# Kernel tuning notes

Measured on AMD Instinct MI355X. Metric: run time of the kernel, lower is better.

Reference implementation:

```python
import jax, jax.numpy as jnp
import numpy as np

N = 50000      # nodes
E = 800000     # edges (before self loops)
IN = 256       # in_dim
HID = 32       # hidden_dim per head
H = 8          # heads layer 1
OUT = 64       # out_dim (classes)
NEG_SLOPE = 0.2  # PyG GATConv default


def gat_conv(x, ei, W, a_src, a_dst, b, heads, ch, concat):
    """PyG GATConv (eval mode, self-loops already in ei).
    x: [n, f_in], ei: [2, e] (row0=src j, row1=dst i), W: [f_in, heads*ch],
    a_src/a_dst: [heads, ch], b: [heads*ch] or [ch]."""
    n = x.shape[0]
    h = (x @ W).reshape(n, heads, ch)                      # [n, H, C]
    src, dst = ei[0], ei[1]
    alpha_src = (h * a_src).sum(-1)                        # [n, H]
    alpha_dst = (h * a_dst).sum(-1)                        # [n, H]
    e = jax.nn.leaky_relu(alpha_src[src] + alpha_dst[dst], NEG_SLOPE)  # [e, H]
    # segment softmax over incoming edges of each dst node
    emax = jax.lax.stop_gradient(jax.ops.segment_max(e, dst, num_segments=n))
    p = jnp.exp(e - emax[dst])
    denom = jax.ops.segment_sum(p, dst, num_segments=n)    # [n, H] (>0: self loops)
    alpha = p / denom[dst]                                 # [e, H]
    out = jax.ops.segment_sum(h[src] * alpha[:, :, None], dst, num_segments=n)  # [n, H, C]
    out = out.reshape(n, heads * ch) if concat else out.mean(axis=1)
    return out + b


def setup_inputs() -> dict:
    key = jax.random.key(0)
    ks = jax.random.split(key, 9)
    x = jax.random.normal(ks[0], (N, IN), jnp.float32)
    edge_index = jax.random.randint(ks[1], (2, E), 0, N, jnp.int32)
    W1 = jax.random.normal(ks[2], (IN, H * HID), jnp.float32) * 0.05
    a_src1 = jax.random.normal(ks[3], (H, HID), jnp.float32) * 0.1
    a_dst1 = jax.random.normal(ks[4], (H, HID), jnp.float32) * 0.1
    b1 = jnp.zeros((H * HID,), jnp.float32)
    W2 = jax.random.normal(ks[5], (H * HID, OUT), jnp.float32) * 0.05
    a_src2 = jax.random.normal(ks[6], (1, OUT), jnp.float32) * 0.1
    a_dst2 = jax.random.normal(ks[7], (1, OUT), jnp.float32) * 0.1
    b2 = jnp.zeros((OUT,), jnp.float32)
    return {"x": x, "edge_index": edge_index, "W1": W1, "a_src1": a_src1,
            "a_dst1": a_dst1, "b1": b1, "W2": W2, "a_src2": a_src2,
            "a_dst2": a_dst2, "b2": b2}


def reference(x, edge_index, W1, a_src1, a_dst1, b1, W2, a_src2, a_dst2, b2):
    n = x.shape[0]
    loops = jnp.arange(n, dtype=edge_index.dtype)
    ei = jnp.concatenate([edge_index, jnp.stack([loops, loops])], axis=1)  # add self loops
    h = gat_conv(x, ei, W1, a_src1, a_dst1, b1, H, HID, concat=True)
    h = jax.nn.relu(h)
    h = gat_conv(h, ei, W2, a_src2, a_dst2, b2, 1, OUT, concat=False)
    return jax.nn.log_softmax(h, axis=1)
```

## Files before the change

### kernel.cpp

```cpp
#include <hip/hip_runtime.h>
#include <math.h>

#define NNODES 50000
#define EORIG  800000
#define ETOT   850000
#define NBUCK  196
#define BSTRIDE 5120
#define P2CHUNK 4096
#define NBLK2  ((ETOT + P2CHUNK - 1)/P2CHUNK)

typedef __attribute__((ext_vector_type(8))) short bf8_t;
typedef __attribute__((ext_vector_type(4))) float f4_t;
typedef __attribute__((ext_vector_type(2))) float f2_t;

constexpr float LOG2E = 1.44269504f;

constexpr size_t align256(size_t x){ return (x + 255) & ~size_t(255); }
constexpr size_t OFF_OFFSETS = 0;
constexpr size_t OFF_DEG     = OFF_OFFSETS + align256((size_t)NNODES*4);
constexpr size_t OFF_GCUR    = OFF_DEG     + align256((size_t)NNODES*4);
constexpr size_t OFF_EPACK   = OFF_GCUR    + align256(NBUCK*4);
constexpr size_t OFF_SRC     = OFF_EPACK   + align256((size_t)NBUCK*BSTRIDE*4);
constexpr size_t OFF_AS1     = OFF_SRC     + align256((size_t)NBUCK*BSTRIDE*4);
constexpr size_t OFF_AD1     = OFF_AS1     + align256((size_t)NNODES*8*4);
constexpr size_t OFF_W1T     = OFF_AD1     + align256((size_t)NNODES*8*4);
constexpr size_t OFF_W2T     = OFF_W1T     + align256(256*256*2);
constexpr size_t OFF_H1F8    = OFF_W2T     + align256(64*256*2);
constexpr size_t OFF_OUT1B   = OFF_H1F8    + align256((size_t)NNODES*256);
constexpr size_t OFF_H2B     = OFF_H1F8;
constexpr size_t OFF_AS2     = OFF_OUT1B   + align256((size_t)NNODES*256*2);
constexpr size_t OFF_AD2     = OFF_AS2     + align256((size_t)NNODES*4);

__device__ __forceinline__ unsigned short f2bf(float f){
    union { float f; unsigned u; } v; v.f = f;
    unsigned r = v.u + 0x7FFF + ((v.u >> 16) & 1);
    return (unsigned short)(r >> 16);
}
__device__ __forceinline__ float bf2f(unsigned short s){
    union { unsigned u; float f; } v; v.u = ((unsigned)s) << 16;
    return v.f;
}


__global__ __launch_bounds__(256) void p3_part(const int* __restrict__ ei, int* __restrict__ gcur,
                                               int* __restrict__ epack){
    __shared__ int h[NBUCK];
    __shared__ int r[NBUCK];
    const int t = threadIdx.x;
    for (int i = t; i < NBUCK; i += 256){ h[i] = 0; r[i] = 0; }
    __syncthreads();
    const int base = blockIdx.x * P2CHUNK;
    int srcs[P2CHUNK/256], dsts[P2CHUNK/256];
#pragma unroll
    for (int j = 0; j < P2CHUNK/256; j++){
        int e = base + j*256 + t;
        if (e < ETOT){
            if (e < EORIG){ srcs[j] = ei[e]; dsts[j] = ei[EORIG + e]; }
            else          { srcs[j] = dsts[j] = e - EORIG; }
            atomicAdd(&h[dsts[j] >> 8], 1);
        } else dsts[j] = -1;
    }
    __syncthreads();
    for (int i = t; i < NBUCK; i += 256){
        int c = h[i];
        h[i] = c ? atomicAdd(&gcur[i], c) : 0;
    }
    __syncthreads();
#pragma unroll
    for (int j = 0; j < P2CHUNK/256; j++){
        if (dsts[j] >= 0){
            int b = dsts[j] >> 8;
            int rk = atomicAdd(&r[b], 1);
            epack[h[b] + rk] = (srcs[j] << 8) | (dsts[j] & 255);
        }
    }
}

__global__ __launch_bounds__(256) void p4_csr(const int* __restrict__ gcur, const int* __restrict__ epack,
                                              int* __restrict__ offsets, int* __restrict__ deg_g,
                                              int* __restrict__ srclist){
    __shared__ int deg[256];
    __shared__ int sm[256];
    __shared__ int cur[256];
    const int b = blockIdx.x, t = threadIdx.x;
    const int s0 = b * BSTRIDE, s1 = gcur[b];
    deg[t] = 0; __syncthreads();
    for (int i = s0 + t; i < s1; i += 256) atomicAdd(&deg[epack[i] & 255], 1);
    __syncthreads();
    int v = deg[t];
    sm[t] = v; __syncthreads();
    for (int off = 1; off < 256; off <<= 1){
        int add = (t >= off) ? sm[t-off] : 0;
        __syncthreads();
        sm[t] += add;
        __syncthreads();
    }
    int excl = sm[t] - v;
    int node = (b << 8) + t;
    if (node < NNODES){ offsets[node] = s0 + excl; deg_g[node] = v; }
    cur[t] = s0 + excl;
    __syncthreads();
    for (int i = s0 + t; i < s1; i += 256){
        int p = epack[i];
        int pos = atomicAdd(&cur[p & 255], 1);
        srclist[pos] = p >> 8;
    }
}


__global__ __launch_bounds__(256) void conv_w_k(const float* __restrict__ W1, const float* __restrict__ W2,
                                                short* __restrict__ w1t, short* __restrict__ w2t,
                                                int* __restrict__ gcur){
    int o = blockIdx.x*256 + threadIdx.x;
    if (o < NBUCK) gcur[o] = o * BSTRIDE;
    if (o < 256*256){
        int n = o >> 8, k = o & 255;
        w1t[o] = (short)f2bf(W1[k*256 + n]);
    } else {
        int o2 = o - 256*256;
        if (o2 < 64*256){
            int n = o2 >> 8, k = o2 & 255;
            w2t[o2] = (short)f2bf(W2[k*64 + n]);
        }
    }
}


__global__ __launch_bounds__(512) void gemm1_mfma(const float* __restrict__ x, const short* __restrict__ w1t,
        const float* __restrict__ a1s, const float* __restrict__ a1d,
        unsigned char* __restrict__ h1f8, float* __restrict__ as1, float* __restrict__ ad1){
    __shared__ short As[128][40];
    __shared__ short Bs[256][40];
    const int t = threadIdx.x;
    const int lane = t & 63, wave = t >> 6;
    const int wy = wave >> 2, wx = wave & 3;
    const int quad = lane >> 4, l15 = lane & 15;
    const int r0 = blockIdx.x * 128;
    const int srow = t >> 2, skoff = (t & 3) * 8;
    f4_t zero4 = {0.f,0.f,0.f,0.f};
    f4_t acc[4][4];
#pragma unroll
    for (int i=0;i<4;i++)
#pragma unroll
      for (int j=0;j<4;j++) acc[i][j] = zero4;

    for (int kk = 0; kk < 256; kk += 32){
        float4 xa0 = {0,0,0,0}, xa1 = {0,0,0,0};
        if (r0 + srow < NNODES){
            xa0 = *(const float4*)(x + (size_t)(r0+srow)*256 + kk + skoff);
            xa1 = *(const float4*)(x + (size_t)(r0+srow)*256 + kk + skoff + 4);
        }
        bf8_t b0  = *(const bf8_t*)(w1t + (size_t)(srow      )*256 + kk + skoff);
        bf8_t b1v = *(const bf8_t*)(w1t + (size_t)(srow + 128)*256 + kk + skoff);
        bf8_t a0;
        a0[0]=f2bf(xa0.x); a0[1]=f2bf(xa0.y); a0[2]=f2bf(xa0.z); a0[3]=f2bf(xa0.w);
        a0[4]=f2bf(xa1.x); a0[5]=f2bf(xa1.y); a0[6]=f2bf(xa1.z); a0[7]=f2bf(xa1.w);
        __syncthreads();
        *(bf8_t*)&As[srow     ][skoff] = a0;
        *(bf8_t*)&Bs[srow     ][skoff] = b0;
        *(bf8_t*)&Bs[srow+128][skoff] = b1v;
        __syncthreads();
        bf8_t af[4], bfr[4];
#pragma unroll
        for (int i=0;i<4;i++) af[i]  = *(const bf8_t*)&As[wy*64 + i*16 + l15][quad*8];
#pragma unroll
        for (int j=0;j<4;j++) bfr[j] = *(const bf8_t*)&Bs[wx*64 + j*16 + l15][quad*8];
#pragma unroll
        for (int i=0;i<4;i++)
#pragma unroll
          for (int j=0;j<4;j++)
            acc[i][j] = __builtin_amdgcn_mfma_f32_16x16x32_bf16(af[i], bfr[j], acc[i][j], 0,0,0);
    }
    const int colbase = wx*64;
    const int head0 = colbase >> 5;
    float cs[4], cd[4];
#pragma unroll
    for (int j=0;j<4;j++){
        cs[j] = a1s[colbase + j*16 + l15] * LOG2E;
        cd[j] = a1d[colbase + j*16 + l15] * LOG2E;
    }
#pragma unroll
    for (int i=0;i<4;i++){
        int rowb = r0 + wy*64 + i*16 + quad*4;
#pragma unroll
        for (int reg=0; reg<4; reg++){
            int row = rowb + reg;
            bool valid = row < NNODES;
            float sp0=0.f, dp0=0.f, sp1=0.f, dp1=0.f;
#pragma unroll
            for (int j=0;j<4;j++){
                float v = acc[i][j][reg];
                if (j < 2){ sp0 += v*cs[j]; dp0 += v*cd[j]; }
                else      { sp1 += v*cs[j]; dp1 += v*cd[j]; }
                if (valid){
                    unsigned enc = (unsigned)__builtin_amdgcn_cvt_pk_fp8_f32(v, v, 0, false);
                    h1f8[(size_t)row*256 + colbase + j*16 + l15] = (unsigned char)(enc & 0xffu);
                }
            }
            sp0 += __shfl_xor(sp0,1); sp0 += __shfl_xor(sp0,2); sp0 += __shfl_xor(sp0,4); sp0 += __shfl_xor(sp0,8);
            dp0 += __shfl_xor(dp0,1); dp0 += __shfl_xor(dp0,2); dp0 += __shfl_xor(dp0,4); dp0 += __shfl_xor(dp0,8);
            sp1 += __shfl_xor(sp1,1); sp1 += __shfl_xor(sp1,2); sp1 += __shfl_xor(sp1,4); sp1 += __shfl_xor(sp1,8);
            dp1 += __shfl_xor(dp1,1); dp1 += __shfl_xor(dp1,2); dp1 += __shfl_xor(dp1,4); dp1 += __shfl_xor(dp1,8);
            if (valid && l15 == 0){
                as1[row*8 + head0    ] = sp0;
                ad1[row*8 + head0    ] = dp0;
                as1[row*8 + head0 + 1] = sp1;
                ad1[row*8 + head0 + 1] = dp1;
            }
        }
    }
}


__global__ __launch_bounds__(256) void gemm2_mfma(const short* __restrict__ ab, const short* __restrict__ w2t,
        const float* __restrict__ a2s, const float* __restrict__ a2d,
        short* __restrict__ h2b, float* __restrict__ as2, float* __restrict__ ad2){
    __shared__ short As[128][40];
    __shared__ short Bs[64][40];
    const int t = threadIdx.x;
    const int lane = t & 63, wave = t >> 6;
    const int quad = lane >> 4, l15 = lane & 15;
    const int r0 = blockIdx.x * 128;
    const int srow = t >> 2, skoff = (t & 3) * 8;
    f4_t zero4 = {0.f,0.f,0.f,0.f};
    f4_t acc[2][4];
#pragma unroll
    for (int i=0;i<2;i++)
#pragma unroll
      for (int j=0;j<4;j++) acc[i][j] = zero4;

    for (int kk = 0; kk < 256; kk += 32){
        bf8_t a0 = {}, a1v = {};
        if (r0 + srow < NNODES)      a0  = *(const bf8_t*)(ab + (size_t)(r0+srow)*256 + kk + skoff);
        if (r0 + srow + 64 < NNODES) a1v = *(const bf8_t*)(ab + (size_t)(r0+srow+64)*256 + kk + skoff);
        bf8_t b0 = *(const bf8_t*)(w2t + (size_t)srow*256 + kk + skoff);
        __syncthreads();
        *(bf8_t*)&As[srow   ][skoff] = a0;
        *(bf8_t*)&As[srow+64][skoff] = a1v;
        *(bf8_t*)&Bs[srow   ][skoff] = b0;
        __syncthreads();
        bf8_t af[2], bfr[4];
#pragma unroll
        for (int i=0;i<2;i++) af[i]  = *(const bf8_t*)&As[wave*32 + i*16 + l15][quad*8];
#pragma unroll
        for (int j=0;j<4;j++) bfr[j] = *(const bf8_t*)&Bs[j*16 + l15][quad*8];
#pragma unroll
        for (int i=0;i<2;i++)
#pragma unroll
          for (int j=0;j<4;j++)
            acc[i][j] = __builtin_amdgcn_mfma_f32_16x16x32_bf16(af[i], bfr[j], acc[i][j], 0,0,0);
    }
    float cs[4], cd[4];
#pragma unroll
    for (int j=0;j<4;j++){
        cs[j] = a2s[j*16 + l15] * LOG2E;
        cd[j] = a2d[j*16 + l15] * LOG2E;
    }
#pragma unroll
    for (int i=0;i<2;i++){
        int rowb = r0 + wave*32 + i*16 + quad*4;
#pragma unroll
        for (int reg=0; reg<4; reg++){
            int row = rowb + reg;
            bool valid = row < NNODES;
            float sp=0.f, dp=0.f;
#pragma unroll
            for (int j=0;j<4;j++){
                float v = acc[i][j][reg];
                sp += v*cs[j]; dp += v*cd[j];
                if (valid) h2b[(size_t)row*64 + j*16 + l15] = (short)f2bf(v);
            }
            sp += __shfl_xor(sp,1); sp += __shfl_xor(sp,2); sp += __shfl_xor(sp,4); sp += __shfl_xor(sp,8);
            dp += __shfl_xor(dp,1); dp += __shfl_xor(dp,2); dp += __shfl_xor(dp,4); dp += __shfl_xor(dp,8);
            if (valid && l15 == 0){ as2[row] = sp; ad2[row] = dp; }
        }
    }
}


__global__ __launch_bounds__(256) void aggregate1_k(const unsigned char* __restrict__ h1f8,
        const float* __restrict__ as1, const float* __restrict__ ad1,
        const int* __restrict__ offsets, const int* __restrict__ deg_g,
        const int* __restrict__ srclist,
        const float* __restrict__ b1, short* __restrict__ out1b){
    int d = blockIdx.x*4 + (threadIdx.x >> 6);
    int lane = threadIdx.x & 63;
    if (d >= NNODES) return;
    const int head_g = lane >> 3;
    const int head_p = lane & 7;
    const int ep     = lane >> 3;
    int start = offsets[d];
    int deg = deg_g[d];
    float ad_p = ad1[d*8 + head_p];
    float denom = 0.f;
    f2_t acc01 = {0.f,0.f}, acc23 = {0.f,0.f};
    for (int w = 0; w < deg; w += 64){
        int deg_w = min(64, deg - w);
        int s_reg = srclist[start + w + min(lane, deg_w-1)];
        int ngr = (deg_w + 7) >> 3;
        auto comp_p = [&](int g)->float{
            int ei = g*8 + ep;
            int s  = __shfl(s_reg, min(ei, deg_w-1));
            float e = as1[s*8 + head_p] + ad_p;
            e = fmaxf(0.2f*e, e);
            float p = exp2f(e);
            return (ei < deg_w) ? p : 0.f;
        };
        float p_reg = comp_p(0);
        for (int g = 0; g < ngr; g++){
            float p_cur = p_reg;
            if (g + 1 < ngr) p_reg = comp_p(g+1);
#pragma unroll
            for (int e = 0; e < 8; e++){
                float pe = __shfl(p_cur, e*8 + head_g);
                int   se = __shfl(s_reg, g*8 + e);
                unsigned wv = *(const unsigned*)(h1f8 + (size_t)se*256 + lane*4);
                f2_t lo = __builtin_amdgcn_cvt_pk_f32_fp8(wv, false);
                f2_t hi = __builtin_amdgcn_cvt_pk_f32_fp8(wv, true);
                acc01 += pe*lo;
                acc23 += pe*hi;
                denom += pe;
            }
        }
    }
    float inv = 1.f / denom;
    float4 bv = *(const float4*)(b1 + lane*4);
    ushort4 us;
    us.x = f2bf(fmaxf(acc01[0]*inv + bv.x, 0.f));
    us.y = f2bf(fmaxf(acc01[1]*inv + bv.y, 0.f));
    us.z = f2bf(fmaxf(acc23[0]*inv + bv.z, 0.f));
    us.w = f2bf(fmaxf(acc23[1]*inv + bv.w, 0.f));
    *(ushort4*)(out1b + (size_t)d*256 + lane*4) = us;
}

__global__ __launch_bounds__(256) void aggregate2_k(const unsigned short* __restrict__ h2b,
        const float* __restrict__ as2, const float* __restrict__ ad2,
        const int* __restrict__ offsets, const int* __restrict__ deg_g,
        const int* __restrict__ srclist,
        const float* __restrict__ b2, float* __restrict__ out){
    int d = blockIdx.x*4 + (threadIdx.x >> 6);
    int lane = threadIdx.x & 63;
    if (d >= NNODES) return;
    int start = offsets[d];
    int deg = deg_g[d];
    float ad_v = ad2[d];
    float denom = 0.f, acc = 0.f;
    for (int w = 0; w < deg; w += 64){
        int deg_w = min(64, deg - w);
        int s_reg = srclist[start + w + min(lane, deg_w-1)];
        float ev = as2[s_reg] + ad_v;
        ev = fmaxf(0.2f*ev, ev);
        float p_lane = (lane < deg_w) ? exp2f(ev) : 0.f;
        int ngr = (deg_w + 7) >> 3;
        for (int g = 0; g < ngr; g++){
#pragma unroll
            for (int e2 = 0; e2 < 8; e2++){
                int ee = g*8 + e2;
                float pe = __shfl(p_lane, ee);
                int   se = __shfl(s_reg, ee);
                float hv = bf2f(h2b[(size_t)se*64 + lane]);
                acc += pe*hv;
                denom += pe;
            }
        }
    }
    float v = acc/denom + b2[lane];
    float mx = v;
#pragma unroll
    for (int off = 1; off < 64; off <<= 1) mx = fmaxf(mx, __shfl_xor(mx, off));
    float ex = __expf(v - mx);
    float ss = ex;
#pragma unroll
    for (int off = 1; off < 64; off <<= 1) ss += __shfl_xor(ss, off);
    out[(size_t)d*64 + lane] = v - mx - __logf(ss);
}


extern "C" void kernel_launch(void* const* d_in, const int* in_sizes, int n_in,
                              void* d_out, int out_size, void* d_ws, size_t ws_size,
                              hipStream_t stream){
    const float* x      = (const float*)d_in[0];
    const int*   ei     = (const int*)  d_in[1];
    const float* W1     = (const float*)d_in[2];
    const float* a_src1 = (const float*)d_in[3];
    const float* a_dst1 = (const float*)d_in[4];
    const float* b1     = (const float*)d_in[5];
    const float* W2     = (const float*)d_in[6];
    const float* a_src2 = (const float*)d_in[7];
    const float* a_dst2 = (const float*)d_in[8];
    const float* b2     = (const float*)d_in[9];

    char* ws = (char*)d_ws;
    int*   offsets = (int*)  (ws + OFF_OFFSETS);
    int*   deg_g   = (int*)  (ws + OFF_DEG);
    int*   gcur    = (int*)  (ws + OFF_GCUR);
    int*   epack   = (int*)  (ws + OFF_EPACK);
    int*   srclist = (int*)  (ws + OFF_SRC);
    float* as1     = (float*)(ws + OFF_AS1);
    float* ad1     = (float*)(ws + OFF_AD1);
    short* w1t     = (short*)(ws + OFF_W1T);
    short* w2t     = (short*)(ws + OFF_W2T);
    unsigned char* h1f8 = (unsigned char*)(ws + OFF_H1F8);
    short* out1b   = (short*)(ws + OFF_OUT1B);
    short* h2b     = (short*)(ws + OFF_H2B);
    float* as2     = (float*)(ws + OFF_AS2);
    float* ad2     = (float*)(ws + OFF_AD2);

    conv_w_k<<<(256*256 + 64*256 + 255)/256, 256, 0, stream>>>(W1, W2, w1t, w2t, gcur);

    p3_part<<<NBLK2, 256, 0, stream>>>(ei, gcur, epack);
    p4_csr <<<NBUCK, 256, 0, stream>>>(gcur, epack, offsets, deg_g, srclist);

    gemm1_mfma<<<(NNODES+127)/128, 512, 0, stream>>>(x, w1t, a_src1, a_dst1, h1f8, as1, ad1);
    aggregate1_k<<<(NNODES+3)/4, 256, 0, stream>>>(h1f8, as1, ad1, offsets, deg_g, srclist, b1, out1b);

    gemm2_mfma<<<(NNODES+127)/128, 256, 0, stream>>>(out1b, w2t, a_src2, a_dst2, h2b, as2, ad2);
    aggregate2_k<<<(NNODES+3)/4, 256, 0, stream>>>((const unsigned short*)h2b, as2, ad2, offsets, deg_g, srclist, b2, (float*)d_out);
}
```

Before: 249.4 us.

## Process two edges per wave step in aggregation kernels and fuse weight conversion into partition

Both aggregation kernels now split each wave into two half-waves. Each half handles a different edge per step and loads wider vectors per lane: 8 fp8 values in layer 1 and 2 bf16 values in layer 2. The two halves are combined with a cross-half shuffle at the end. Separately, the weight transpose/convert kernel is merged into the edge partition kernel as extra blocks, and the bucket cursor is reset with a memset. This removes one launch and changes the cursor to a relative offset. The aim is fewer serial gather iterations and wider memory transactions, at the cost of a final reduction and more per-step shuffles.

```diff
diff --git a/kernel.cpp b/kernel.cpp
--- a/kernel.cpp
+++ b/kernel.cpp
@@ -8,8 +8,10 @@
 #define BSTRIDE 5120
 #define P2CHUNK 4096
 #define NBLK2  ((ETOT + P2CHUNK - 1)/P2CHUNK)
+#define NBLKW  ((256*256 + 64*256 + 255)/256)
 
 typedef __attribute__((ext_vector_type(8))) short bf8_t;
+typedef __attribute__((ext_vector_type(8))) unsigned short us8_t;
 typedef __attribute__((ext_vector_type(4))) float f4_t;
 typedef __attribute__((ext_vector_type(2))) float f2_t;
 
@@ -42,11 +44,27 @@
 }
 
 
-__global__ __launch_bounds__(256) void p3_part(const int* __restrict__ ei, int* __restrict__ gcur,
-                                               int* __restrict__ epack){
+__global__ __launch_bounds__(256) void prep_k(const int* __restrict__ ei, int* __restrict__ gcur,
+                                              int* __restrict__ epack,
+                                              const float* __restrict__ W1, const float* __restrict__ W2,
+                                              short* __restrict__ w1t, short* __restrict__ w2t){
+    const int t = threadIdx.x;
+    if (blockIdx.x >= NBLK2){
+        int o = (blockIdx.x - NBLK2)*256 + t;
+        if (o < 256*256){
+            int n = o >> 8, k = o & 255;
+            w1t[o] = (short)f2bf(W1[k*256 + n]);
+        } else {
+            int o2 = o - 256*256;
+            if (o2 < 64*256){
+                int n = o2 >> 8, k = o2 & 255;
+                w2t[o2] = (short)f2bf(W2[k*64 + n]);
+            }
+        }
+        return;
+    }
     __shared__ int h[NBUCK];
     __shared__ int r[NBUCK];
-    const int t = threadIdx.x;
     for (int i = t; i < NBUCK; i += 256){ h[i] = 0; r[i] = 0; }
     __syncthreads();
     const int base = blockIdx.x * P2CHUNK;
@@ -63,7 +81,7 @@
     __syncthreads();
     for (int i = t; i < NBUCK; i += 256){
         int c = h[i];
-        h[i] = c ? atomicAdd(&gcur[i], c) : 0;
+        h[i] = c ? (i*BSTRIDE + atomicAdd(&gcur[i], c)) : 0;
     }
     __syncthreads();
 #pragma unroll
@@ -83,7 +101,7 @@
     __shared__ int sm[256];
     __shared__ int cur[256];
     const int b = blockIdx.x, t = threadIdx.x;
-    const int s0 = b * BSTRIDE, s1 = gcur[b];
+    const int s0 = b * BSTRIDE, s1 = s0 + gcur[b];
     deg[t] = 0; __syncthreads();
     for (int i = s0 + t; i < s1; i += 256) atomicAdd(&deg[epack[i] & 255], 1);
     __syncthreads();
@@ -104,24 +122,6 @@
         int p = epack[i];
         int pos = atomicAdd(&cur[p & 255], 1);
         srclist[pos] = p >> 8;
-    }
-}
-
-
-__global__ __launch_bounds__(256) void conv_w_k(const float* __restrict__ W1, const float* __restrict__ W2,
-                                                short* __restrict__ w1t, short* __restrict__ w2t,
-                                                int* __restrict__ gcur){
-    int o = blockIdx.x*256 + threadIdx.x;
-    if (o < NBUCK) gcur[o] = o * BSTRIDE;
-    if (o < 256*256){
-        int n = o >> 8, k = o & 255;
-        w1t[o] = (short)f2bf(W1[k*256 + n]);
-    } else {
-        int o2 = o - 256*256;
-        if (o2 < 64*256){
-            int n = o2 >> 8, k = o2 & 255;
-            w2t[o2] = (short)f2bf(W2[k*64 + n]);
-        }
     }
 }
 
@@ -286,22 +286,25 @@
     int d = blockIdx.x*4 + (threadIdx.x >> 6);
     int lane = threadIdx.x & 63;
     if (d >= NNODES) return;
-    const int head_g = lane >> 3;
-    const int head_p = lane & 7;
-    const int ep     = lane >> 3;
+    const int q      = lane & 31;
+    const int epair  = lane >> 5;
+    const int head_q = q >> 2;
+    const int p_head = lane & 7;
+    const int p_edge = (lane >> 3) & 1;
+    const int psrc   = (epair << 3) | head_q;
     int start = offsets[d];
     int deg = deg_g[d];
-    float ad_p = ad1[d*8 + head_p];
+    float ad_p = ad1[d*8 + p_head];
     float denom = 0.f;
-    f2_t acc01 = {0.f,0.f}, acc23 = {0.f,0.f};
+    f2_t a0={0,0}, a1={0,0}, a2={0,0}, a3={0,0};
     for (int w = 0; w < deg; w += 64){
         int deg_w = min(64, deg - w);
         int s_reg = srclist[start + w + min(lane, deg_w-1)];
-        int ngr = (deg_w + 7) >> 3;
+        int ngr = (deg_w + 1) >> 1;
         auto comp_p = [&](int g)->float{
-            int ei = g*8 + ep;
+            int ei = g*2 + p_edge;
             int s  = __shfl(s_reg, min(ei, deg_w-1));
-            float e = as1[s*8 + head_p] + ad_p;
+            float e = as1[s*8 + p_head] + ad_p;
             e = fmaxf(0.2f*e, e);
             float p = exp2f(e);
             return (ei < deg_w) ? p : 0.f;
@@ -310,27 +313,38 @@
         for (int g = 0; g < ngr; g++){
             float p_cur = p_reg;
             if (g + 1 < ngr) p_reg = comp_p(g+1);
-#pragma unroll
-            for (int e = 0; e < 8; e++){
-                float pe = __shfl(p_cur, e*8 + head_g);
-                int   se = __shfl(s_reg, g*8 + e);
-                unsigned wv = *(const unsigned*)(h1f8 + (size_t)se*256 + lane*4);
-                f2_t lo = __builtin_amdgcn_cvt_pk_f32_fp8(wv, false);
-                f2_t hi = __builtin_amdgcn_cvt_pk_f32_fp8(wv, true);
-                acc01 += pe*lo;
-                acc23 += pe*hi;
-                denom += pe;
-            }
-        }
-    }
-    float inv = 1.f / denom;
-    float4 bv = *(const float4*)(b1 + lane*4);
-    ushort4 us;
-    us.x = f2bf(fmaxf(acc01[0]*inv + bv.x, 0.f));
-    us.y = f2bf(fmaxf(acc01[1]*inv + bv.y, 0.f));
-    us.z = f2bf(fmaxf(acc23[0]*inv + bv.z, 0.f));
-    us.w = f2bf(fmaxf(acc23[1]*inv + bv.w, 0.f));
-    *(ushort4*)(out1b + (size_t)d*256 + lane*4) = us;
+            int ei = g*2 + epair;
+            int se = __shfl(s_reg, min(ei, deg_w-1));
+            float pe = __shfl(p_cur, psrc);
+            uint2 wv = *(const uint2*)(h1f8 + (size_t)se*256 + q*8);
+            f2_t lo0 = __builtin_amdgcn_cvt_pk_f32_fp8(wv.x, false);
+            f2_t hi0 = __builtin_amdgcn_cvt_pk_f32_fp8(wv.x, true);
+            f2_t lo1 = __builtin_amdgcn_cvt_pk_f32_fp8(wv.y, false);
+            f2_t hi1 = __builtin_amdgcn_cvt_pk_f32_fp8(wv.y, true);
+            a0 += pe*lo0; a1 += pe*hi0; a2 += pe*lo1; a3 += pe*hi1;
+            denom += pe;
+        }
+    }
+    a0[0] += __shfl_xor(a0[0], 32); a0[1] += __shfl_xor(a0[1], 32);
+    a1[0] += __shfl_xor(a1[0], 32); a1[1] += __shfl_xor(a1[1], 32);
+    a2[0] += __shfl_xor(a2[0], 32); a2[1] += __shfl_xor(a2[1], 32);
+    a3[0] += __shfl_xor(a3[0], 32); a3[1] += __shfl_xor(a3[1], 32);
+    denom += __shfl_xor(denom, 32);
+    if (lane < 32){
+        float inv = 1.f / denom;
+        float4 bv0 = *(const float4*)(b1 + q*8);
+        float4 bv1 = *(const float4*)(b1 + q*8 + 4);
+        us8_t us;
+        us[0] = f2bf(fmaxf(a0[0]*inv + bv0.x, 0.f));
+        us[1] = f2bf(fmaxf(a0[1]*inv + bv0.y, 0.f));
+        us[2] = f2bf(fmaxf(a1[0]*inv + bv0.z, 0.f));
+        us[3] = f2bf(fmaxf(a1[1]*inv + bv0.w, 0.f));
+        us[4] = f2bf(fmaxf(a2[0]*inv + bv1.x, 0.f));
+        us[5] = f2bf(fmaxf(a2[1]*inv + bv1.y, 0.f));
+        us[6] = f2bf(fmaxf(a3[0]*inv + bv1.z, 0.f));
+        us[7] = f2bf(fmaxf(a3[1]*inv + bv1.w, 0.f));
+        *(us8_t*)(out1b + (size_t)d*256 + q*8) = us;
+    }
 }
 
 __global__ __launch_bounds__(256) void aggregate2_k(const unsigned short* __restrict__ h2b,
@@ -341,38 +355,48 @@
     int d = blockIdx.x*4 + (threadIdx.x >> 6);
     int lane = threadIdx.x & 63;
     if (d >= NNODES) return;
+    const int q     = lane & 31;
+    const int epair = lane >> 5;
     int start = offsets[d];
     int deg = deg_g[d];
     float ad_v = ad2[d];
-    float denom = 0.f, acc = 0.f;
+    float denom = 0.f;
+    f2_t acc = {0.f, 0.f};
     for (int w = 0; w < deg; w += 64){
         int deg_w = min(64, deg - w);
         int s_reg = srclist[start + w + min(lane, deg_w-1)];
         float ev = as2[s_reg] + ad_v;
         ev = fmaxf(0.2f*ev, ev);
         float p_lane = (lane < deg_w) ? exp2f(ev) : 0.f;
-        int ngr = (deg_w + 7) >> 3;
+        int ngr = (deg_w + 1) >> 1;
         for (int g = 0; g < ngr; g++){
-#pragma unroll
-            for (int e2 = 0; e2 < 8; e2++){
-                int ee = g*8 + e2;
-                float pe = __shfl(p_lane, ee);
-                int   se = __shfl(s_reg, ee);
-                float hv = bf2f(h2b[(size_t)se*64 + lane]);
-                acc += pe*hv;
-                denom += pe;
-            }
-        }
-    }
-    float v = acc/denom + b2[lane];
-    float mx = v;
-#pragma unroll
-    for (int off = 1; off < 64; off <<= 1) mx = fmaxf(mx, __shfl_xor(mx, off));
-    float ex = __expf(v - mx);
-    float ss = ex;
-#pragma unroll
-    for (int off = 1; off < 64; off <<= 1) ss += __shfl_xor(ss, off);
-    out[(size_t)d*64 + lane] = v - mx - __logf(ss);
+            int ei = g*2 + epair;
+            float pe = __shfl(p_lane, min(ei, 63));
+            int   se = __shfl(s_reg, min(ei, deg_w-1));
+            unsigned u = *(const unsigned*)(h2b + (size_t)se*64 + q*2);
+            f2_t hv = { bf2f((unsigned short)(u & 0xffffu)), bf2f((unsigned short)(u >> 16)) };
+            acc += pe*hv;
+            denom += pe;
+        }
+    }
+    acc[0] += __shfl_xor(acc[0], 32);
+    acc[1] += __shfl_xor(acc[1], 32);
+    denom  += __shfl_xor(denom, 32);
+    float inv = 1.f / denom;
+    float2 bvv = *(const float2*)(b2 + q*2);
+    float v0 = acc[0]*inv + bvv.x;
+    float v1 = acc[1]*inv + bvv.y;
+    float mx = fmaxf(v0, v1);
+#pragma unroll
+    for (int off = 1; off < 32; off <<= 1) mx = fmaxf(mx, __shfl_xor(mx, off));
+    float ss = __expf(v0 - mx) + __expf(v1 - mx);
+#pragma unroll
+    for (int off = 1; off < 32; off <<= 1) ss += __shfl_xor(ss, off);
+    float lg = mx + __logf(ss);
+    if (lane < 32){
+        float2 o = { v0 - lg, v1 - lg };
+        *(float2*)(out + (size_t)d*64 + q*2) = o;
+    }
 }
 
 
@@ -406,10 +430,9 @@
     float* as2     = (float*)(ws + OFF_AS2);
     float* ad2     = (float*)(ws + OFF_AD2);
 
-    conv_w_k<<<(256*256 + 64*256 + 255)/256, 256, 0, stream>>>(W1, W2, w1t, w2t, gcur);
-
-    p3_part<<<NBLK2, 256, 0, stream>>>(ei, gcur, epack);
-    p4_csr <<<NBUCK, 256, 0, stream>>>(gcur, epack, offsets, deg_g, srclist);
+    hipMemsetAsync(gcur, 0, NBUCK*sizeof(int), stream);
+    prep_k<<<NBLK2 + NBLKW, 256, 0, stream>>>(ei, gcur, epack, W1, W2, w1t, w2t);
+    p4_csr<<<NBUCK, 256, 0, stream>>>(gcur, epack, offsets, deg_g, srclist);
 
     gemm1_mfma<<<(NNODES+127)/128, 512, 0, stream>>>(x, w1t, a_src1, a_dst1, h1f8, as1, ad1);
     aggregate1_k<<<(NNODES+3)/4, 256, 0, stream>>>(h1f8, as1, ad1, offsets, deg_g, srclist, b1, out1b);
```

Result: slower. 279.5 us (+12.0%).
